# Kernel optimization log

Hardware: AMD Instinct MI355X
Metric: run time of the kernel (lower is better)

## Reference

```python
import jax, jax.numpy as jnp
import numpy as np

HID = 2048
NH = 16
HD = HID // NH  # 128
THETA = 10000.0


def _rope_cos_sin(position_ids):
    # inv_freq: [HD/2]
    inv_freq = 1.0 / (THETA ** (jnp.arange(0, HD, 2, dtype=jnp.float32) / HD))
    freqs = position_ids.astype(jnp.float32)[:, :, None] * inv_freq[None, None, :]  # [b,s,hd/2]
    emb = jnp.concatenate([freqs, freqs], axis=-1)  # [b,s,hd]
    return jnp.cos(emb), jnp.sin(emb)


def _rotate_half(x):
    x1, x2 = x[..., : HD // 2], x[..., HD // 2:]
    return jnp.concatenate([-x2, x1], axis=-1)


def setup_inputs() -> dict:
    key = jax.random.key(0)
    ks = jax.random.split(key, 10)
    b, s = 2, 2048
    scale = 1.0 / np.sqrt(HID)
    hidden_states = jax.random.normal(ks[0], (b, s, HID), dtype=jnp.float32)
    wq = jax.random.normal(ks[1], (HID, HID), dtype=jnp.float32) * scale
    wk = jax.random.normal(ks[2], (HID, HID), dtype=jnp.float32) * scale
    wv = jax.random.normal(ks[3], (HID, HID), dtype=jnp.float32) * scale
    wo = jax.random.normal(ks[4], (HID, HID), dtype=jnp.float32) * scale
    bq = jnp.zeros((HID,), jnp.float32)
    bk = jnp.zeros((HID,), jnp.float32)
    bv = jnp.zeros((HID,), jnp.float32)
    bo = jnp.zeros((HID,), jnp.float32)
    # HF-style additive causal mask [b,1,q,kv]: 0 on/below diag, large negative above
    neg = jnp.finfo(jnp.float32).min
    causal = jnp.where(jnp.tril(jnp.ones((s, s), dtype=bool)), 0.0, neg)
    attention_mask = jnp.broadcast_to(causal[None, None], (b, 1, s, s)).astype(jnp.float32)
    position_ids = jnp.broadcast_to(jnp.arange(s, dtype=jnp.int32)[None], (b, s))
    return {
        "hidden_states": hidden_states,
        "wq": wq, "bq": bq, "wk": wk, "bk": bk,
        "wv": wv, "bv": bv, "wo": wo, "bo": bo,
        "attention_mask": attention_mask, "position_ids": position_ids,
    }


def reference(hidden_states, wq, bq, wk, bk, wv, bv, wo, bo, attention_mask, position_ids):
    b, s, _ = hidden_states.shape
    q = hidden_states @ wq.T + bq  # [b,s,hid]
    k = hidden_states @ wk.T + bk
    v = hidden_states @ wv.T + bv
    # [b, nh, s, hd]
    q = q.reshape(b, s, NH, HD).transpose(0, 2, 1, 3)
    k = k.reshape(b, s, NH, HD).transpose(0, 2, 1, 3)
    v = v.reshape(b, s, NH, HD).transpose(0, 2, 1, 3)
    cos, sin = _rope_cos_sin(position_ids)  # [b,s,hd]
    cos, sin = cos[:, None], sin[:, None]  # unsqueeze_dim=1 -> [b,1,s,hd]
    q = q * cos + _rotate_half(q) * sin
    k = k * cos + _rotate_half(k) * sin
    scores = jnp.einsum("bhqd,bhkd->bhqk", q, k) / np.sqrt(HD)
    scores = scores + attention_mask
    attn = jax.nn.softmax(scores.astype(jnp.float32), axis=-1).astype(q.dtype)
    out = jnp.einsum("bhqk,bhkd->bhqd", attn, v)  # [b,nh,s,hd]
    out = out.transpose(0, 2, 1, 3).reshape(b, s, HID)
    return out @ wo.T + bo
```

## Files before the change

kernel.cpp:

```cpp
#include <hip/hip_runtime.h>

#define S_LEN 2048
#define HID   2048
#define NHEAD 16
#define HDIM  128
#define BATCH 2
#define KDIM  2048

using bf16x8  = __attribute__((ext_vector_type(8))) short;
using f32x4   = __attribute__((ext_vector_type(4))) float;
using short4v = __attribute__((ext_vector_type(4))) short;

__device__ __forceinline__ short f2bf(float f) {
  union { float f; unsigned u; } v; v.f = f;
  unsigned r = v.u + 0x7fffu + ((v.u >> 16) & 1u);
  return (short)(r >> 16);
}
__device__ __forceinline__ float bf2f(short s) {
  union { unsigned u; float f; } v;
  v.u = ((unsigned)(unsigned short)s) << 16;
  return v.f;
}

__device__ __forceinline__ void gl_lds16(const void* g, void* l) {
  __builtin_amdgcn_global_load_lds(
      (const __attribute__((address_space(1))) void*)g,
      (__attribute__((address_space(3))) void*)l, 16, 0, 0);
}

__global__ __launch_bounds__(256)
void convert_all(const float* __restrict__ hs, const float* __restrict__ wq,
                 const float* __restrict__ wk, const float* __restrict__ wv,
                 const float* __restrict__ wo,
                 short* __restrict__ hsb, short* __restrict__ wqkv,
                 short* __restrict__ wob)
{
  const int base = blockIdx.x * 256 + threadIdx.x;
#pragma unroll
  for (int it = 0; it < 6; ++it) {
    int j = base + it * 524288;
    const float* src; short* dst;
    if (j < 1048576)      { src = hs; dst = hsb; }
    else if (j < 1572864) { j -= 1048576; src = wq; dst = wqkv; }
    else if (j < 2097152) { j -= 1572864; src = wk; dst = wqkv + 4194304; }
    else if (j < 2621440) { j -= 2097152; src = wv; dst = wqkv + 8388608; }
    else                  { j -= 2621440; src = wo; dst = wob; }
    f32x4 a = ((const f32x4*)src)[2 * j];
    f32x4 b = ((const f32x4*)src)[2 * j + 1];
    bf16x8 o;
    o[0]=f2bf(a[0]); o[1]=f2bf(a[1]); o[2]=f2bf(a[2]); o[3]=f2bf(a[3]);
    o[4]=f2bf(b[0]); o[5]=f2bf(b[1]); o[6]=f2bf(b[2]); o[7]=f2bf(b[3]);
    ((bf16x8*)dst)[j] = o;
  }
}

template<int KIND>
__global__ __launch_bounds__(256)
void gemm128(const short* __restrict__ A, const short* __restrict__ B,
             const float* __restrict__ bias0, const float* __restrict__ bias1,
             const float* __restrict__ bias2,
             void* __restrict__ O0, void* __restrict__ O1, void* __restrict__ O2)
{
  __shared__ __align__(16) short As[128 * 64];
  __shared__ __align__(16) short Bs[128 * 64];
  const int tid  = threadIdx.x;
  const int lane = tid & 63, wave = tid >> 6;
  const int ln = lane & 15, g = lane >> 4;
  const int wr = wave >> 1, wc = wave & 1;
  const int m0 = blockIdx.x * 128, n0 = blockIdx.y * 128;

  const int srow   = tid >> 3;
  const int schunk = (tid & 7) ^ (srow & 7);
  const short* aS = A + (size_t)(m0 + srow) * KDIM + schunk * 8;
  const short* bS = B + (size_t)(n0 + srow) * KDIM + schunk * 8;

  f32x4 acc[4][4] = {};

  for (int k0 = 0; k0 < KDIM; k0 += 64) {
    __syncthreads();
#pragma unroll
    for (int j = 0; j < 4; ++j) {
      gl_lds16(aS + k0 + j * (32 * KDIM), &As[j * 2048 + tid * 8]);
      gl_lds16(bS + k0 + j * (32 * KDIM), &Bs[j * 2048 + tid * 8]);
    }
    __syncthreads();

#pragma unroll
    for (int ks = 0; ks < 2; ++ks) {
      bf16x8 af[4], bfm[4];
#pragma unroll
      for (int i = 0; i < 4; ++i) {
        const int r = wr * 64 + i * 16 + ln;
        af[i] = *(const bf16x8*)&As[r * 64 + (((ks * 4 + g) ^ (r & 7)) << 3)];
      }
#pragma unroll
      for (int j2 = 0; j2 < 4; ++j2) {
        const int r = wc * 64 + j2 * 16 + ln;
        bfm[j2] = *(const bf16x8*)&Bs[r * 64 + (((ks * 4 + g) ^ (r & 7)) << 3)];
      }
#pragma unroll
      for (int i = 0; i < 4; ++i)
#pragma unroll
        for (int j2 = 0; j2 < 4; ++j2)
          acc[i][j2] = __builtin_amdgcn_mfma_f32_16x16x32_bf16(af[i], bfm[j2], acc[i][j2], 0, 0, 0);
    }
  }

  if constexpr (KIND == 0) {
    const int seg   = n0 >> 11;
    const int nbase = (n0 & 2047) + wc * 64;
    const float* bias = (seg == 0) ? bias0 : (seg == 1) ? bias1 : bias2;
    float bvv[4];
#pragma unroll
    for (int j = 0; j < 4; ++j) bvv[j] = bias[nbase + j * 16 + ln];
    if (seg < 2) {
      short* C = (short*)(seg ? O1 : O0);
#pragma unroll
      for (int i = 0; i < 4; ++i) {
        const int mb = m0 + wr * 64 + i * 16 + 4 * g;
#pragma unroll
        for (int j = 0; j < 4; ++j) {
          const int nl = nbase + j * 16 + ln;
          const int h = nl >> 7, d = nl & 127;
#pragma unroll
          for (int e = 0; e < 4; ++e) {
            const int m = mb + e, bb = m >> 11, t = m & (S_LEN - 1);
            C[((size_t)((bb * NHEAD + h) * S_LEN + t) << 7) + d] = f2bf(acc[i][j][e] + bvv[j]);
          }
        }
      }
    } else {
      short* C = (short*)O2;
#pragma unroll
      for (int i = 0; i < 4; ++i) {
        const int mb = m0 + wr * 64 + i * 16 + 4 * g;
        const int bb = mb >> 11, t0 = mb & (S_LEN - 1);
#pragma unroll
        for (int j = 0; j < 4; ++j) {
          const int nl = nbase + j * 16 + ln;
          const int h = nl >> 7, d = nl & 127;
          short4v v;
#pragma unroll
          for (int e = 0; e < 4; ++e) v[e] = f2bf(acc[i][j][e] + bvv[j]);
          *(short4v*)&C[((size_t)((bb * NHEAD + h) * HDIM + d)) * S_LEN + t0] = v;
        }
      }
    }
  } else {
    float* C = (float*)O0;
    float bvv[4];
#pragma unroll
    for (int j = 0; j < 4; ++j) bvv[j] = bias0[n0 + wc * 64 + j * 16 + ln];
#pragma unroll
    for (int i = 0; i < 4; ++i) {
      const int mb = m0 + wr * 64 + i * 16 + 4 * g;
#pragma unroll
      for (int j = 0; j < 4; ++j) {
        const int n = n0 + wc * 64 + j * 16 + ln;
#pragma unroll
        for (int e = 0; e < 4; ++e)
          C[(size_t)(mb + e) * HID + n] = acc[i][j][e] + bvv[j];
      }
    }
  }
}

#define QSCALE 0.12752767502f
__global__ __launch_bounds__(256)
void rope_kernel(short* __restrict__ Qb, short* __restrict__ Kb,
                 const int* __restrict__ pos_ids)
{
  const int row = blockIdx.x * 4 + (threadIdx.x >> 6);
  const int d   = threadIdx.x & 63;
  const int bh  = row >> 11, t = row & (S_LEN - 1);
  const int b   = bh >> 4;
  const float pos = (float)pos_ids[b * S_LEN + t];
  const float inv = exp2f((float)d * -0.20762050593f);
  float s, c;
  sincosf(pos * inv, &s, &c);
  const size_t base = (size_t)row * HDIM;
  {
    float x1 = bf2f(Qb[base + d]), x2 = bf2f(Qb[base + d + 64]);
    Qb[base + d]      = f2bf((x1 * c - x2 * s) * QSCALE);
    Qb[base + d + 64] = f2bf((x2 * c + x1 * s) * QSCALE);
  }
  {
    float x1 = bf2f(Kb[base + d]), x2 = bf2f(Kb[base + d + 64]);
    Kb[base + d]      = f2bf(x1 * c - x2 * s);
    Kb[base + d + 64] = f2bf(x2 * c + x1 * s);
  }
}

__global__ __launch_bounds__(512)
void attn_kernel(const short* __restrict__ Qb, const short* __restrict__ Kb,
                 const short* __restrict__ Vt, short* __restrict__ AO)
{
  __shared__ __align__(16) short Ks[128 * 128];
  __shared__ __align__(16) short Vs[128 * 128];
  __shared__ __align__(16) short Ps[8][16 * 64];
  const int tid  = threadIdx.x;
  const int wave = tid >> 6, lane = tid & 63;
  const int ln = lane & 15, g = lane >> 4;
  const int bid = blockIdx.x;
  const int bh  = bid & 31;
  const int grp = bid >> 5;
  const int yt  = (grp & 7) ^ ((grp & 8) ? 15 : 0);
  const int qw  = yt * 128 + wave * 16;

  const short* Kbh = Kb + (size_t)bh * (S_LEN * HDIM);
  const short* Vbh = Vt + (size_t)bh * (S_LEN * HDIM);
  const int sOff = (tid >> 4) * 0 + ((((tid & 15) ^ ((tid >> 4) & 7))) << 3);
  const int kOff = (tid >> 4) * HDIM  + sOff;
  const int vOff = (tid >> 4) * S_LEN + sOff;

  bf16x8 qf[4];
#pragma unroll
  for (int ks = 0; ks < 4; ++ks)
    qf[ks] = *(const bf16x8*)&Qb[((size_t)bh * S_LEN + qw + ln) * HDIM + ks * 32 + g * 8];

  f32x4 o[8] = {};
  float m_e[4], l_e[4];
#pragma unroll
  for (int e = 0; e < 4; ++e) { m_e[e] = -3.0e38f; l_e[e] = 0.f; }

  for (int kvt = 0; kvt <= yt; ++kvt) {
    const int kv0 = kvt * 128;
    __syncthreads();
#pragma unroll
    for (int p = 0; p < 4; ++p) {
      gl_lds16(Kbh + (size_t)kv0 * HDIM + kOff + p * (32 * HDIM),
               &Ks[p * 4096 + tid * 8]);
      gl_lds16(Vbh + kv0 + vOff + p * (32 * S_LEN),
               &Vs[p * 4096 + tid * 8]);
    }
    __syncthreads();

    for (int h = 0; h < 2; ++h) {
      const int kvb = kv0 + h * 64;

      f32x4 sfr[4] = {};
      __builtin_amdgcn_s_setprio(1);
#pragma unroll
      for (int ks = 0; ks < 4; ++ks) {
#pragma unroll
        for (int nt = 0; nt < 4; ++nt) {
          const int row = h * 64 + nt * 16 + ln;
          bf16x8 kf = *(const bf16x8*)&Ks[(row * 128 + ks * 32 + g * 8) ^ ((row & 7) << 3)];
          sfr[nt] = __builtin_amdgcn_mfma_f32_16x16x32_bf16(qf[ks], kf, sfr[nt], 0, 0, 0);
        }
      }
      __builtin_amdgcn_s_setprio(0);

      float rmax_e[4];
#pragma unroll
      for (int e = 0; e < 4; ++e) {
        const int q = qw + 4 * g + e;
        float rmax = -3.0e38f;
#pragma unroll
        for (int nt = 0; nt < 4; ++nt) {
          float v = sfr[nt][e];
          if (kvb + nt * 16 + ln > q) v = -3.0e38f;
          sfr[nt][e] = v;
          rmax = fmaxf(rmax, v);
        }
#pragma unroll
        for (int msk = 1; msk < 16; msk <<= 1)
          rmax = fmaxf(rmax, __shfl_xor(rmax, msk));
        rmax_e[e] = rmax;
      }

      bool grow = false;
#pragma unroll
      for (int e = 0; e < 4; ++e) grow |= (rmax_e[e] > m_e[e] + 8.0f);
      if (__any(grow)) {
#pragma unroll
        for (int e = 0; e < 4; ++e) {
          const float nm = fmaxf(m_e[e], rmax_e[e]);
          const float corr = exp2f(m_e[e] - nm);
          m_e[e] = nm;
          l_e[e] *= corr;
#pragma unroll
          for (int nt2 = 0; nt2 < 8; ++nt2) o[nt2][e] *= corr;
        }
      }

#pragma unroll
      for (int e = 0; e < 4; ++e) {
        float psum = 0.f;
#pragma unroll
        for (int nt = 0; nt < 4; ++nt) {
          const float pv = exp2f(sfr[nt][e] - m_e[e]);
          sfr[nt][e] = pv;
          psum += pv;
        }
        l_e[e] += psum;
      }

      short* pw = &Ps[wave][0];
#pragma unroll
      for (int e = 0; e < 4; ++e) {
        const int r = 4 * g + e;
#pragma unroll
        for (int nt = 0; nt < 4; ++nt) {
          const int cc = nt * 16 + ln;
          pw[(r * 64 + cc) ^ ((r & 7) << 3)] = f2bf(sfr[nt][e]);
        }
      }
      asm volatile("s_waitcnt lgkmcnt(0)" ::: "memory");
      __builtin_amdgcn_sched_barrier(0);

      __builtin_amdgcn_s_setprio(1);
#pragma unroll
      for (int ks2 = 0; ks2 < 2; ++ks2) {
        bf16x8 pa = *(const bf16x8*)&pw[(ln * 64 + ks2 * 32 + g * 8) ^ ((ln & 7) << 3)];
#pragma unroll
        for (int nt2 = 0; nt2 < 8; ++nt2) {
          const int row = nt2 * 16 + ln;
          bf16x8 vb = *(const bf16x8*)&Vs[(row * 128 + h * 64 + ks2 * 32 + g * 8) ^ ((row & 7) << 3)];
          o[nt2] = __builtin_amdgcn_mfma_f32_16x16x32_bf16(pa, vb, o[nt2], 0, 0, 0);
        }
      }
      __builtin_amdgcn_s_setprio(0);
    }
  }

  const int b = bh >> 4, h2 = bh & 15;
#pragma unroll
  for (int e = 0; e < 4; ++e) {
    float l = l_e[e];
#pragma unroll
    for (int msk = 1; msk < 16; msk <<= 1)
      l += __shfl_xor(l, msk);
    const float inv = 1.0f / l;
    const int q = qw + 4 * g + e;
    short* dst = &AO[((size_t)b * S_LEN + q) * HID + h2 * HDIM];
#pragma unroll
    for (int nt2 = 0; nt2 < 8; ++nt2)
      dst[nt2 * 16 + ln] = f2bf(o[nt2][e] * inv);
  }
}

extern "C" void kernel_launch(void* const* d_in, const int* in_sizes, int n_in,
                              void* d_out, int out_size, void* d_ws, size_t ws_size,
                              hipStream_t stream)
{
  const float* hs = (const float*)d_in[0];
  const float* wq = (const float*)d_in[1];
  const float* bq = (const float*)d_in[2];
  const float* wk = (const float*)d_in[3];
  const float* bk = (const float*)d_in[4];
  const float* wv = (const float*)d_in[5];
  const float* bv = (const float*)d_in[6];
  const float* wo = (const float*)d_in[7];
  const float* bo = (const float*)d_in[8];
  const int*  pos = (const int*)d_in[10];
  float* out = (float*)d_out;

  const size_t TSZ = (size_t)BATCH * NHEAD * S_LEN * HDIM;
  short* Qb   = (short*)d_ws;
  short* Kb   = Qb + TSZ;
  short* Vt   = Kb + TSZ;
  short* hsb  = Vt + TSZ;
  short* AO   = hsb;
  short* Wqkv = hsb + TSZ;
  short* wob  = Wqkv + 12582912;

  convert_all<<<2048, 256, 0, stream>>>(hs, wq, wk, wv, wo, hsb, Wqkv, wob);
  gemm128<0><<<dim3(32, 48), 256, 0, stream>>>(hsb, Wqkv, bq, bk, bv, Qb, Kb, Vt);
  rope_kernel<<<(BATCH * NHEAD * S_LEN) / 4, 256, 0, stream>>>(Qb, Kb, pos);
  attn_kernel<<<512, 512, 0, stream>>>(Qb, Kb, Vt, AO);
  gemm128<1><<<dim3(32, 16), 256, 0, stream>>>(AO, wob, bo, nullptr, nullptr, out, nullptr, nullptr);
}
```

Measured before the change: 273.0 us.

## Rewrite attention with 32x32 MFMA transposed scores and in-register P

Switches the flash-attention kernel from 16x16x32 to 32x32x16 bf16 MFMA, computing S^T = K·Q^T so each lane owns one query row. P is converted to bf16 in registers with cvt_pk and permlane32_swap instead of going through an LDS scratch buffer. The kernel now runs 4 waves of 32 queries per block instead of 8 waves of 16, and causal masking applies only on the diagonal tile. This cuts LDS round trips, shuffles and per-row reductions, at the cost of fewer waves per block and higher register pressure.

```diff
diff --git a/kernel.cpp b/kernel.cpp
--- a/kernel.cpp
+++ b/kernel.cpp
@@ -9,7 +9,9 @@
 
 using bf16x8  = __attribute__((ext_vector_type(8))) short;
 using f32x4   = __attribute__((ext_vector_type(4))) float;
+using f32x16  = __attribute__((ext_vector_type(16))) float;
 using short4v = __attribute__((ext_vector_type(4))) short;
+using uint4v  = __attribute__((ext_vector_type(4))) unsigned;
 
 __device__ __forceinline__ short f2bf(float f) {
   union { float f; unsigned u; } v; v.f = f;
@@ -191,152 +193,143 @@
   }
 }
 
-__global__ __launch_bounds__(512)
+__global__ __launch_bounds__(256)
 void attn_kernel(const short* __restrict__ Qb, const short* __restrict__ Kb,
                  const short* __restrict__ Vt, short* __restrict__ AO)
 {
   __shared__ __align__(16) short Ks[128 * 128];
   __shared__ __align__(16) short Vs[128 * 128];
-  __shared__ __align__(16) short Ps[8][16 * 64];
   const int tid  = threadIdx.x;
   const int wave = tid >> 6, lane = tid & 63;
-  const int ln = lane & 15, g = lane >> 4;
+  const int lq = lane & 31, lh = lane >> 5;
   const int bid = blockIdx.x;
   const int bh  = bid & 31;
   const int grp = bid >> 5;
   const int yt  = (grp & 7) ^ ((grp & 8) ? 15 : 0);
-  const int qw  = yt * 128 + wave * 16;
+  const int qw  = yt * 128 + wave * 32;
+  const int q   = qw + lq;
 
   const short* Kbh = Kb + (size_t)bh * (S_LEN * HDIM);
   const short* Vbh = Vt + (size_t)bh * (S_LEN * HDIM);
-  const int sOff = (tid >> 4) * 0 + ((((tid & 15) ^ ((tid >> 4) & 7))) << 3);
-  const int kOff = (tid >> 4) * HDIM  + sOff;
-  const int vOff = (tid >> 4) * S_LEN + sOff;
-
-  bf16x8 qf[4];
-#pragma unroll
-  for (int ks = 0; ks < 4; ++ks)
-    qf[ks] = *(const bf16x8*)&Qb[((size_t)bh * S_LEN + qw + ln) * HDIM + ks * 32 + g * 8];
-
-  f32x4 o[8] = {};
-  float m_e[4], l_e[4];
-#pragma unroll
-  for (int e = 0; e < 4; ++e) { m_e[e] = -3.0e38f; l_e[e] = 0.f; }
+  const int sw   = ((tid & 15) ^ ((tid >> 4) & 7)) << 3;
+  const int kOff = (tid >> 4) * HDIM + sw;
+  const int vOff = (tid >> 4) * S_LEN + sw;
+
+  bf16x8 qf[8];
+#pragma unroll
+  for (int kk = 0; kk < 8; ++kk)
+    qf[kk] = *(const bf16x8*)&Qb[((size_t)bh * S_LEN + q) * HDIM + kk * 16 + lh * 8];
+
+  f32x16 o[4] = {};
+  float m_s = -3.0e38f, l_s = 0.f;
 
   for (int kvt = 0; kvt <= yt; ++kvt) {
     const int kv0 = kvt * 128;
     __syncthreads();
 #pragma unroll
-    for (int p = 0; p < 4; ++p) {
-      gl_lds16(Kbh + (size_t)kv0 * HDIM + kOff + p * (32 * HDIM),
-               &Ks[p * 4096 + tid * 8]);
-      gl_lds16(Vbh + kv0 + vOff + p * (32 * S_LEN),
-               &Vs[p * 4096 + tid * 8]);
+    for (int p = 0; p < 8; ++p) {
+      gl_lds16(Kbh + (size_t)kv0 * HDIM + kOff + p * (16 * HDIM), &Ks[p * 2048 + tid * 8]);
+      gl_lds16(Vbh + kv0 + vOff + p * (16 * S_LEN),               &Vs[p * 2048 + tid * 8]);
     }
     __syncthreads();
 
+#pragma unroll
     for (int h = 0; h < 2; ++h) {
-      const int kvb = kv0 + h * 64;
-
-      f32x4 sfr[4] = {};
+      f32x16 sfr[2] = {};
       __builtin_amdgcn_s_setprio(1);
 #pragma unroll
-      for (int ks = 0; ks < 4; ++ks) {
-#pragma unroll
-        for (int nt = 0; nt < 4; ++nt) {
-          const int row = h * 64 + nt * 16 + ln;
-          bf16x8 kf = *(const bf16x8*)&Ks[(row * 128 + ks * 32 + g * 8) ^ ((row & 7) << 3)];
-          sfr[nt] = __builtin_amdgcn_mfma_f32_16x16x32_bf16(qf[ks], kf, sfr[nt], 0, 0, 0);
+      for (int kk = 0; kk < 8; ++kk) {
+#pragma unroll
+        for (int nt = 0; nt < 2; ++nt) {
+          const int row = h * 64 + nt * 32 + lq;
+          bf16x8 ak = *(const bf16x8*)&Ks[(row * 128 + kk * 16 + lh * 8) ^ ((row & 7) << 3)];
+          sfr[nt] = __builtin_amdgcn_mfma_f32_32x32x16_bf16(ak, qf[kk], sfr[nt], 0, 0, 0);
         }
       }
       __builtin_amdgcn_s_setprio(0);
 
-      float rmax_e[4];
-#pragma unroll
-      for (int e = 0; e < 4; ++e) {
-        const int q = qw + 4 * g + e;
-        float rmax = -3.0e38f;
-#pragma unroll
-        for (int nt = 0; nt < 4; ++nt) {
-          float v = sfr[nt][e];
-          if (kvb + nt * 16 + ln > q) v = -3.0e38f;
-          sfr[nt][e] = v;
-          rmax = fmaxf(rmax, v);
-        }
-#pragma unroll
-        for (int msk = 1; msk < 16; msk <<= 1)
-          rmax = fmaxf(rmax, __shfl_xor(rmax, msk));
-        rmax_e[e] = rmax;
-      }
-
-      bool grow = false;
-#pragma unroll
-      for (int e = 0; e < 4; ++e) grow |= (rmax_e[e] > m_e[e] + 8.0f);
-      if (__any(grow)) {
-#pragma unroll
-        for (int e = 0; e < 4; ++e) {
-          const float nm = fmaxf(m_e[e], rmax_e[e]);
-          const float corr = exp2f(m_e[e] - nm);
-          m_e[e] = nm;
-          l_e[e] *= corr;
-#pragma unroll
-          for (int nt2 = 0; nt2 < 8; ++nt2) o[nt2][e] *= corr;
-        }
-      }
-
-#pragma unroll
-      for (int e = 0; e < 4; ++e) {
-        float psum = 0.f;
-#pragma unroll
-        for (int nt = 0; nt < 4; ++nt) {
-          const float pv = exp2f(sfr[nt][e] - m_e[e]);
-          sfr[nt][e] = pv;
-          psum += pv;
-        }
-        l_e[e] += psum;
-      }
-
-      short* pw = &Ps[wave][0];
-#pragma unroll
-      for (int e = 0; e < 4; ++e) {
-        const int r = 4 * g + e;
-#pragma unroll
-        for (int nt = 0; nt < 4; ++nt) {
-          const int cc = nt * 16 + ln;
-          pw[(r * 64 + cc) ^ ((r & 7) << 3)] = f2bf(sfr[nt][e]);
-        }
-      }
-      asm volatile("s_waitcnt lgkmcnt(0)" ::: "memory");
-      __builtin_amdgcn_sched_barrier(0);
+      if (kvt == yt) {
+#pragma unroll
+        for (int nt = 0; nt < 2; ++nt) {
+          const int kvb = kv0 + h * 64 + nt * 32 + 4 * lh;
+#pragma unroll
+          for (int r = 0; r < 16; ++r) {
+            const int kv = kvb + (r & 3) + 8 * (r >> 2);
+            if (kv > q) sfr[nt][r] = -3.0e38f;
+          }
+        }
+      }
+      float rmax = -3.0e38f;
+#pragma unroll
+      for (int nt = 0; nt < 2; ++nt)
+#pragma unroll
+        for (int r = 0; r < 16; ++r) rmax = fmaxf(rmax, sfr[nt][r]);
+      rmax = fmaxf(rmax, __shfl_xor(rmax, 32));
+
+      if (__any(rmax > m_s + 8.0f)) {
+        const float nm = fmaxf(m_s, rmax);
+        const float corr = exp2f(m_s - nm);
+        m_s = nm;
+        l_s *= corr;
+#pragma unroll
+        for (int dt = 0; dt < 4; ++dt)
+#pragma unroll
+          for (int r = 0; r < 16; ++r) o[dt][r] *= corr;
+      }
+
+      float ps = 0.f;
+#pragma unroll
+      for (int nt = 0; nt < 2; ++nt)
+#pragma unroll
+        for (int r = 0; r < 16; ++r) {
+          const float pv = exp2f(sfr[nt][r] - m_s);
+          sfr[nt][r] = pv;
+          ps += pv;
+        }
+      l_s += ps;
+
+      bf16x8 pa[4];
+#pragma unroll
+      for (int kk = 0; kk < 4; ++kk) {
+        const int nt = kk >> 1, c8 = (kk & 1) * 8;
+        unsigned w0, w1, w2, w3;
+        asm("v_cvt_pk_bf16_f32 %0, %1, %2" : "=v"(w0) : "v"(sfr[nt][c8 + 0]), "v"(sfr[nt][c8 + 1]));
+        asm("v_cvt_pk_bf16_f32 %0, %1, %2" : "=v"(w1) : "v"(sfr[nt][c8 + 2]), "v"(sfr[nt][c8 + 3]));
+        asm("v_cvt_pk_bf16_f32 %0, %1, %2" : "=v"(w2) : "v"(sfr[nt][c8 + 4]), "v"(sfr[nt][c8 + 5]));
+        asm("v_cvt_pk_bf16_f32 %0, %1, %2" : "=v"(w3) : "v"(sfr[nt][c8 + 6]), "v"(sfr[nt][c8 + 7]));
+        asm volatile("v_permlane32_swap_b32 %0, %1" : "+v"(w0), "+v"(w2));
+        asm volatile("v_permlane32_swap_b32 %0, %1" : "+v"(w1), "+v"(w3));
+        uint4v u; u[0] = w0; u[1] = w1; u[2] = w2; u[3] = w3;
+        pa[kk] = __builtin_bit_cast(bf16x8, u);
+      }
 
       __builtin_amdgcn_s_setprio(1);
 #pragma unroll
-      for (int ks2 = 0; ks2 < 2; ++ks2) {
-        bf16x8 pa = *(const bf16x8*)&pw[(ln * 64 + ks2 * 32 + g * 8) ^ ((ln & 7) << 3)];
-#pragma unroll
-        for (int nt2 = 0; nt2 < 8; ++nt2) {
-          const int row = nt2 * 16 + ln;
-          bf16x8 vb = *(const bf16x8*)&Vs[(row * 128 + h * 64 + ks2 * 32 + g * 8) ^ ((row & 7) << 3)];
-          o[nt2] = __builtin_amdgcn_mfma_f32_16x16x32_bf16(pa, vb, o[nt2], 0, 0, 0);
+      for (int kk = 0; kk < 4; ++kk) {
+#pragma unroll
+        for (int dt = 0; dt < 4; ++dt) {
+          const int row = dt * 32 + lq;
+          bf16x8 av = *(const bf16x8*)&Vs[(row * 128 + h * 64 + kk * 16 + lh * 8) ^ ((row & 7) << 3)];
+          o[dt] = __builtin_amdgcn_mfma_f32_32x32x16_bf16(av, pa[kk], o[dt], 0, 0, 0);
         }
       }
       __builtin_amdgcn_s_setprio(0);
     }
   }
 
-  const int b = bh >> 4, h2 = bh & 15;
-#pragma unroll
-  for (int e = 0; e < 4; ++e) {
-    float l = l_e[e];
-#pragma unroll
-    for (int msk = 1; msk < 16; msk <<= 1)
-      l += __shfl_xor(l, msk);
-    const float inv = 1.0f / l;
-    const int q = qw + 4 * g + e;
-    short* dst = &AO[((size_t)b * S_LEN + q) * HID + h2 * HDIM];
-#pragma unroll
-    for (int nt2 = 0; nt2 < 8; ++nt2)
-      dst[nt2 * 16 + ln] = f2bf(o[nt2][e] * inv);
+  l_s += __shfl_xor(l_s, 32);
+  const float inv = 1.0f / l_s;
+  const int b = bh >> 4, hh = bh & 15;
+  short* dst = &AO[((size_t)b * S_LEN + q) * HID + hh * HDIM];
+#pragma unroll
+  for (int dt = 0; dt < 4; ++dt) {
+#pragma unroll
+    for (int rq = 0; rq < 4; ++rq) {
+      short4v v4;
+#pragma unroll
+      for (int e = 0; e < 4; ++e) v4[e] = f2bf(o[dt][rq * 4 + e] * inv);
+      *(short4v*)&dst[dt * 32 + rq * 8 + 4 * lh] = v4;
+    }
   }
 }
 
@@ -368,6 +361,6 @@
   convert_all<<<2048, 256, 0, stream>>>(hs, wq, wk, wv, wo, hsb, Wqkv, wob);
   gemm128<0><<<dim3(32, 48), 256, 0, stream>>>(hsb, Wqkv, bq, bk, bv, Qb, Kb, Vt);
   rope_kernel<<<(BATCH * NHEAD * S_LEN) / 4, 256, 0, stream>>>(Qb, Kb, pos);
-  attn_kernel<<<512, 512, 0, stream>>>(Qb, Kb, Vt, AO);
+  attn_kernel<<<512, 256, 0, stream>>>(Qb, Kb, Vt, AO);
   gemm128<1><<<dim3(32, 16), 256, 0, stream>>>(AO, wob, bo, nullptr, nullptr, out, nullptr, nullptr);
 }
```

Result: faster. 254.3 us (-6.8%).
